# Kernel optimization log

Measured on AMD Instinct MI355X. Metric: run time of the kernel, lower is better.

The kernel has to match this reference:

```python
import jax, jax.numpy as jnp
import numpy as np

R = 3  # correlation radius -> (2R+1)^2 = 49 offsets
OFFSETS = [(dy, dx) for dy in range(-R, R + 1) for dx in range(-R, R + 1)]


def local_correlation(f1, f2):
    # f1, f2: [B, C, H, W] -> [B, 49, H, W]
    C = f1.shape[1]
    scale = np.float32(1.0 / np.sqrt(C))
    vols = [jnp.sum(f1 * jnp.roll(f2, (dy, dx), axis=(2, 3)), axis=1)
            for dy, dx in OFFSETS]  # fixed 49-offset structural loop
    return jnp.stack(vols, axis=1) * scale


def _level(lvl, w, b):
    # lvl: [T, B, C, H, W]; correlate consecutive frame pairs
    corr = jax.vmap(local_correlation)(lvl[:-1], lvl[1:])  # [T-1, B, 49, H, W]
    # 1x1 conv == channel contraction: [49, token_dim]
    return jnp.einsum('tbkhw,kd->tbdhw', corr, w) + b[None, None, :, None, None]


def setup_inputs() -> dict:
    key = jax.random.key(0)
    ks = jax.random.split(key, 9)
    T, B = 3, 2
    token_dim, K = 192, 49
    return {
        'l1': jax.random.normal(ks[0], (T, B, 64, 128, 128), jnp.float32),
        'l2': jax.random.normal(ks[1], (T, B, 128, 64, 64), jnp.float32),
        'l3': jax.random.normal(ks[2], (T, B, 192, 32, 32), jnp.float32),
        'w1': jax.random.normal(ks[3], (K, token_dim), jnp.float32) * 0.05,
        'b1': jax.random.normal(ks[4], (token_dim,), jnp.float32) * 0.05,
        'w2': jax.random.normal(ks[5], (K, token_dim), jnp.float32) * 0.05,
        'b2': jax.random.normal(ks[6], (token_dim,), jnp.float32) * 0.05,
        'w3': jax.random.normal(ks[7], (K, token_dim), jnp.float32) * 0.05,
        'b3': jax.random.normal(ks[8], (token_dim,), jnp.float32) * 0.05,
    }


def reference(l1, l2, l3, w1, b1, w2, b2, w3, b3):
    tok1 = _level(l1, w1, b1)  # [T-1, B, 192, 128, 128]
    tok2 = _level(l2, w2, b2)  # [T-1, B, 192, 64, 64]
    tok3 = _level(l3, w3, b3)  # [T-1, B, 192, 32, 32]
    return (tok1, tok2, tok3)
```

## Files before the change

kernel.cpp:

```cpp
#include <hip/hip_runtime.h>


#define TD 192
#define HSTRIDE 26

template<int C, int H, int W, int TX, int TY>
__device__ __forceinline__ void level_tile(
    const float* __restrict__ lvl, const float* __restrict__ wm,
    const float* __restrict__ bias, float* __restrict__ out,
    int r, float scale, float* __restrict__ smem)
{
    const int HW = H * W;
    const int xcd = r & 7, q = r >> 3;
    const int tY  = q % TY;
    const int col = (q / TY) * 8 + xcd;
    const int pair = col / TX, tX = col % TX;

    const int t  = pair >> 1, bb = pair & 1;
    const float* f1 = lvl + (t * 2 + bb) * C * HW;
    const float* f2 = lvl + ((t + 1) * 2 + bb) * C * HW;

    const int tid  = threadIdx.x;
    const int lane = tid & 63;
    const int g    = tid >> 6;
    const int tx   = lane & 15, tyy = lane >> 4;
    const int x0   = tX * 16, y0 = tY * 8;
    const int x    = x0 + tx;
    const int y    = y0 + 2 * tyy;

    float4* h = (float4*)smem + g * (14 * HSTRIDE);

    int goff[5], loff[5];
#pragma unroll
    for (int i = 0; i < 5; ++i) {
        int p = lane + i * 64;
        int rr = p / 22, cc = p - rr * 22;
        int gy = y0 - 3 + rr; if (gy < 0) gy += H; if (gy >= H) gy -= H;
        int gx = x0 - 3 + cc; if (gx < 0) gx += W; if (gx >= W) gx -= W;
        goff[i] = gy * W + gx;
        loff[i] = rr * HSTRIDE + cc;
    }

    float acc0[49], acc1[49];
#pragma unroll
    for (int k = 0; k < 49; ++k) { acc0[k] = 0.f; acc1[k] = 0.f; }

    const int NCH = C / 16;
    const float* f2c = f2 + g * (C / 4) * HW;
    const float* f1c = f1 + g * (C / 4) * HW + y * W + x;
#pragma unroll 1
    for (int cg = 0; cg < NCH; ++cg) {
#pragma unroll
        for (int i = 0; i < 5; ++i) {
            if (i < 4 || lane < 52) {
                const float* s = f2c + goff[i];
                float4 v; v.x = s[0]; v.y = s[HW]; v.z = s[2 * HW]; v.w = s[3 * HW];
                h[loff[i]] = v;
            }
        }
        float a00 = f1c[0], a01 = f1c[HW], a02 = f1c[2 * HW], a03 = f1c[3 * HW];
        float a10 = f1c[W], a11 = f1c[HW + W], a12 = f1c[2 * HW + W], a13 = f1c[3 * HW + W];
        f2c += 4 * HW; f1c += 4 * HW;
#pragma unroll
        for (int b = 0; b < 7; ++b) {
            const float4* hp = h + (2 * tyy) * HSTRIDE + (tx + 6 - b);
            float4 hi = hp[7 * HSTRIDE];
#pragma unroll
            for (int a = 0; a < 7; ++a) {
                float4 lo = hp[(6 - a) * HSTRIDE];
                float s0 = acc0[a * 7 + b], s1 = acc1[a * 7 + b];
                s0 = fmaf(a00, lo.x, s0); s0 = fmaf(a01, lo.y, s0);
                s0 = fmaf(a02, lo.z, s0); s0 = fmaf(a03, lo.w, s0);
                s1 = fmaf(a10, hi.x, s1); s1 = fmaf(a11, hi.y, s1);
                s1 = fmaf(a12, hi.z, s1); s1 = fmaf(a13, hi.w, s1);
                acc0[a * 7 + b] = s0; acc1[a * 7 + b] = s1;
                hi = lo;
            }
        }
    }

    __syncthreads();
    float* s0p = smem;
    float* s1p = smem + 49 * 128;
    if (g >= 2) {
        float* dst = (g == 2) ? s0p : s1p;
#pragma unroll
        for (int k = 0; k < 49; ++k) {
            dst[k * 128 + lane]      = acc0[k];
            dst[k * 128 + 64 + lane] = acc1[k];
        }
    }
    __syncthreads();
    if (g < 2) {
        float* dst = (g == 0) ? s0p : s1p;
#pragma unroll
        for (int k = 0; k < 49; ++k) {
            dst[k * 128 + lane]      += acc0[k];
            dst[k * 128 + 64 + lane] += acc1[k];
        }
    }
    __syncthreads();

    const int dbase = __builtin_amdgcn_readfirstlane(g * 48);
    float sA[48], sB[48];
#pragma unroll
    for (int j = 0; j < 48; ++j) { float bv = bias[dbase + j]; sA[j] = bv; sB[j] = bv; }
#pragma unroll 1
    for (int k = 0; k < 49; ++k) {
        float c0 = (s0p[k * 128 + lane]      + s1p[k * 128 + lane])      * scale;
        float c1 = (s0p[k * 128 + 64 + lane] + s1p[k * 128 + 64 + lane]) * scale;
        const float* wr = wm + k * TD + dbase;
#pragma unroll
        for (int j = 0; j < 48; ++j) {
            float wv = wr[j];
            sA[j] = fmaf(wv, c0, sA[j]);
            sB[j] = fmaf(wv, c1, sB[j]);
        }
    }
    float* op = out + (pair * TD + dbase) * HW + y * W + x;
#pragma unroll
    for (int j = 0; j < 48; ++j) {
        op[j * HW] = sA[j]; op[j * HW + W] = sB[j];
    }
}

__global__ __launch_bounds__(256, 2)
void cost_tokenizer(const float* __restrict__ l1, const float* __restrict__ l2,
                    const float* __restrict__ l3,
                    const float* __restrict__ w1, const float* __restrict__ b1,
                    const float* __restrict__ w2, const float* __restrict__ b2,
                    const float* __restrict__ w3, const float* __restrict__ b3,
                    float* __restrict__ out)
{
    __shared__ __align__(16) float smem[12544];
    int bid = blockIdx.x;
    if (bid < 32) {
        level_tile<192, 32, 32, 2, 4>(l3, w3, b3, out + 15728640,
                                      bid, 0.072168783648703216f, smem);
    } else if (bid < 160) {
        level_tile<128, 64, 64, 4, 8>(l2, w2, b2, out + 12582912,
                                      bid - 32, 0.088388347648318447f, smem);
    } else {
        level_tile<64, 128, 128, 8, 16>(l1, w1, b1, out,
                                        bid - 160, 0.125f, smem);
    }
}

extern "C" void kernel_launch(void* const* d_in, const int* in_sizes, int n_in,
                              void* d_out, int out_size, void* d_ws, size_t ws_size,
                              hipStream_t stream)
{
    const float* l1 = (const float*)d_in[0];
    const float* l2 = (const float*)d_in[1];
    const float* l3 = (const float*)d_in[2];
    const float* w1 = (const float*)d_in[3];
    const float* b1 = (const float*)d_in[4];
    const float* w2 = (const float*)d_in[5];
    const float* b2 = (const float*)d_in[6];
    const float* w3 = (const float*)d_in[7];
    const float* b3 = (const float*)d_in[8];
    float* out = (float*)d_out;

    hipLaunchKernelGGL(cost_tokenizer, dim3(672), dim3(256), 0, stream,
                       l1, l2, l3, w1, b1, w2, b2, w3, b3, out);
}
```

Baseline: 161.0 us.

## Halve per-thread output rows to cut registers and double occupancy

After: 156.0 us. 3.1% less time.

```diff
diff --git a/kernel.cpp b/kernel.cpp
--- a/kernel.cpp
+++ b/kernel.cpp
@@ -23,16 +23,16 @@
     const int tid  = threadIdx.x;
     const int lane = tid & 63;
     const int g    = tid >> 6;
-    const int tx   = lane & 15, tyy = lane >> 4;
-    const int x0   = tX * 16, y0 = tY * 8;
+    const int tx   = lane & 15, ty = lane >> 4;
+    const int x0   = tX * 16, y0 = tY * 4;
     const int x    = x0 + tx;
-    const int y    = y0 + 2 * tyy;
+    const int y    = y0 + ty;
 
-    float4* h = (float4*)smem + g * (14 * HSTRIDE);
+    float4* h = (float4*)smem + g * (10 * HSTRIDE);
 
-    int goff[5], loff[5];
+    int goff[4], loff[4];
 #pragma unroll
-    for (int i = 0; i < 5; ++i) {
+    for (int i = 0; i < 4; ++i) {
         int p = lane + i * 64;
         int rr = p / 22, cc = p - rr * 22;
         int gy = y0 - 3 + rr; if (gy < 0) gy += H; if (gy >= H) gy -= H;
@@ -41,9 +41,9 @@
         loff[i] = rr * HSTRIDE + cc;
     }
 
-    float acc0[49], acc1[49];
+    float acc[49];
 #pragma unroll
-    for (int k = 0; k < 49; ++k) { acc0[k] = 0.f; acc1[k] = 0.f; }
+    for (int k = 0; k < 49; ++k) acc[k] = 0.f;
 
     const int NCH = C / 16;
     const float* f2c = f2 + g * (C / 4) * HW;
@@ -51,80 +51,66 @@
 #pragma unroll 1
     for (int cg = 0; cg < NCH; ++cg) {
 #pragma unroll
-        for (int i = 0; i < 5; ++i) {
-            if (i < 4 || lane < 52) {
+        for (int i = 0; i < 4; ++i) {
+            if (i < 3 || lane < 28) {
                 const float* s = f2c + goff[i];
                 float4 v; v.x = s[0]; v.y = s[HW]; v.z = s[2 * HW]; v.w = s[3 * HW];
                 h[loff[i]] = v;
             }
         }
-        float a00 = f1c[0], a01 = f1c[HW], a02 = f1c[2 * HW], a03 = f1c[3 * HW];
-        float a10 = f1c[W], a11 = f1c[HW + W], a12 = f1c[2 * HW + W], a13 = f1c[3 * HW + W];
+        float a0 = f1c[0], a1 = f1c[HW], a2 = f1c[2 * HW], a3 = f1c[3 * HW];
         f2c += 4 * HW; f1c += 4 * HW;
 #pragma unroll
         for (int b = 0; b < 7; ++b) {
-            const float4* hp = h + (2 * tyy) * HSTRIDE + (tx + 6 - b);
-            float4 hi = hp[7 * HSTRIDE];
+            const float4* hp = h + ty * HSTRIDE + (tx + 6 - b);
 #pragma unroll
             for (int a = 0; a < 7; ++a) {
                 float4 lo = hp[(6 - a) * HSTRIDE];
-                float s0 = acc0[a * 7 + b], s1 = acc1[a * 7 + b];
-                s0 = fmaf(a00, lo.x, s0); s0 = fmaf(a01, lo.y, s0);
-                s0 = fmaf(a02, lo.z, s0); s0 = fmaf(a03, lo.w, s0);
-                s1 = fmaf(a10, hi.x, s1); s1 = fmaf(a11, hi.y, s1);
-                s1 = fmaf(a12, hi.z, s1); s1 = fmaf(a13, hi.w, s1);
-                acc0[a * 7 + b] = s0; acc1[a * 7 + b] = s1;
-                hi = lo;
+                float s0 = acc[a * 7 + b];
+                s0 = fmaf(a0, lo.x, s0); s0 = fmaf(a1, lo.y, s0);
+                s0 = fmaf(a2, lo.z, s0); s0 = fmaf(a3, lo.w, s0);
+                acc[a * 7 + b] = s0;
             }
         }
     }
 
     __syncthreads();
     float* s0p = smem;
-    float* s1p = smem + 49 * 128;
+    float* s1p = smem + 49 * 64;
     if (g >= 2) {
         float* dst = (g == 2) ? s0p : s1p;
 #pragma unroll
-        for (int k = 0; k < 49; ++k) {
-            dst[k * 128 + lane]      = acc0[k];
-            dst[k * 128 + 64 + lane] = acc1[k];
-        }
+        for (int k = 0; k < 49; ++k)
+            dst[k * 64 + lane] = acc[k];
     }
     __syncthreads();
     if (g < 2) {
         float* dst = (g == 0) ? s0p : s1p;
 #pragma unroll
-        for (int k = 0; k < 49; ++k) {
-            dst[k * 128 + lane]      += acc0[k];
-            dst[k * 128 + 64 + lane] += acc1[k];
-        }
+        for (int k = 0; k < 49; ++k)
+            dst[k * 64 + lane] += acc[k];
     }
     __syncthreads();
 
     const int dbase = __builtin_amdgcn_readfirstlane(g * 48);
-    float sA[48], sB[48];
+    float sA[48];
 #pragma unroll
-    for (int j = 0; j < 48; ++j) { float bv = bias[dbase + j]; sA[j] = bv; sB[j] = bv; }
+    for (int j = 0; j < 48; ++j) sA[j] = bias[dbase + j];
 #pragma unroll 1
     for (int k = 0; k < 49; ++k) {
-        float c0 = (s0p[k * 128 + lane]      + s1p[k * 128 + lane])      * scale;
-        float c1 = (s0p[k * 128 + 64 + lane] + s1p[k * 128 + 64 + lane]) * scale;
+        float c0 = (s0p[k * 64 + lane] + s1p[k * 64 + lane]) * scale;
         const float* wr = wm + k * TD + dbase;
 #pragma unroll
-        for (int j = 0; j < 48; ++j) {
-            float wv = wr[j];
-            sA[j] = fmaf(wv, c0, sA[j]);
-            sB[j] = fmaf(wv, c1, sB[j]);
-        }
+        for (int j = 0; j < 48; ++j)
+            sA[j] = fmaf(wr[j], c0, sA[j]);
     }
     float* op = out + (pair * TD + dbase) * HW + y * W + x;
 #pragma unroll
-    for (int j = 0; j < 48; ++j) {
-        op[j * HW] = sA[j]; op[j * HW + W] = sB[j];
-    }
+    for (int j = 0; j < 48; ++j)
+        op[j * HW] = sA[j];
 }
 
-__global__ __launch_bounds__(256, 2)
+__global__ __launch_bounds__(256, 4)
 void cost_tokenizer(const float* __restrict__ l1, const float* __restrict__ l2,
                     const float* __restrict__ l3,
                     const float* __restrict__ w1, const float* __restrict__ b1,
@@ -132,17 +118,17 @@
                     const float* __restrict__ w3, const float* __restrict__ b3,
                     float* __restrict__ out)
 {
-    __shared__ __align__(16) float smem[12544];
+    __shared__ __align__(16) float smem[6272];
     int bid = blockIdx.x;
-    if (bid < 32) {
-        level_tile<192, 32, 32, 2, 4>(l3, w3, b3, out + 15728640,
+    if (bid < 64) {
+        level_tile<192, 32, 32, 2, 8>(l3, w3, b3, out + 15728640,
                                       bid, 0.072168783648703216f, smem);
-    } else if (bid < 160) {
-        level_tile<128, 64, 64, 4, 8>(l2, w2, b2, out + 12582912,
-                                      bid - 32, 0.088388347648318447f, smem);
+    } else if (bid < 320) {
+        level_tile<128, 64, 64, 4, 16>(l2, w2, b2, out + 12582912,
+                                       bid - 64, 0.088388347648318447f, smem);
     } else {
-        level_tile<64, 128, 128, 8, 16>(l1, w1, b1, out,
-                                        bid - 160, 0.125f, smem);
+        level_tile<64, 128, 128, 8, 32>(l1, w1, b1, out,
+                                        bid - 320, 0.125f, smem);
     }
 }
 
@@ -161,6 +147,6 @@
     const float* b3 = (const float*)d_in[8];
     float* out = (float*)d_out;
 
-    hipLaunchKernelGGL(cost_tokenizer, dim3(672), dim3(256), 0, stream,
+    hipLaunchKernelGGL(cost_tokenizer, dim3(1344), dim3(256), 0, stream,
                        l1, l2, l3, w1, b1, w2, b2, w3, b3, out);
 }
```
